# Kernel optimization log

Hardware: AMD Instinct MI355X
Metric: run time of the kernel (lower is better)

The kernel has to match this reference:

```python
import jax, jax.numpy as jnp
import numpy as np

V, D, H, L, F, S_MAX = 32000, 1024, 16, 6, 4, 1024
B, S = 2, 1024
HD = D // H  # head dim = 64


def setup_inputs() -> dict:
    key = jax.random.key(0)
    ks = jax.random.split(key, 8)
    init = lambda k, shape: jax.random.normal(k, shape, jnp.float32) * 0.02
    return dict(
        X=jax.random.randint(ks[0], (B, S), 0, V),
        tok_emb=init(ks[1], (V, D)),
        pos_emb=jnp.zeros((1, S_MAX, D), jnp.float32),  # initialized to zeros as in source
        qkv_w=init(ks[2], (D, 3 * D)), qkv_b=jnp.zeros((3 * D,), jnp.float32),
        out_w=init(ks[3], (D, D)), out_b=jnp.zeros((D,), jnp.float32),
        ln1_s=jnp.ones((D,), jnp.float32), ln1_b=jnp.zeros((D,), jnp.float32),
        ln2_s=jnp.ones((D,), jnp.float32), ln2_b=jnp.zeros((D,), jnp.float32),
        ff1_w=init(ks[4], (D, F * D)), ff1_b=jnp.zeros((F * D,), jnp.float32),
        ff2_w=init(ks[5], (F * D, D)), ff2_b=jnp.zeros((D,), jnp.float32),
        lnf_s=jnp.ones((D,), jnp.float32), lnf_b=jnp.zeros((D,), jnp.float32),
        head_w=init(ks[6], (D, V)), head_b=jnp.zeros((V,), jnp.float32),
    )


def _layernorm(x, scale, bias, eps=1e-5):
    m = x.mean(-1, keepdims=True)
    v = x.var(-1, keepdims=True)
    return (x - m) / jnp.sqrt(v + eps) * scale + bias


def _attention(x, qkv_w, qkv_b, out_w, out_b, mask):
    b, s, _ = x.shape
    qkv = (x @ qkv_w + qkv_b).reshape(b, s, H, 3 * HD)
    q, k, v = jnp.split(qkv, 3, axis=-1)  # each [b,s,H,HD]
    attn = jnp.einsum('bqhd,bkhd->bhqk', q, k) / jnp.sqrt(jnp.float32(HD))
    attn = jnp.where(mask, attn, -jnp.inf)
    attn = jax.nn.softmax(attn, axis=-1)
    out = jnp.einsum('bhqk,bkhd->bqhd', attn, v).reshape(b, s, D)
    return out @ out_w + out_b


def reference(X, tok_emb, pos_emb, qkv_w, qkv_b, out_w, out_b,
              ln1_s, ln1_b, ln2_s, ln2_b, ff1_w, ff1_b, ff2_w, ff2_b,
              lnf_s, lnf_b, head_w, head_b):
    s = X.shape[1]
    x = tok_emb[X] + pos_emb[:, :s, :]
    mask = jnp.tril(jnp.ones((s, s), bool))  # causal
    # NOTE: the source GPT reuses ONE shared GPTBlock for all layers.
    for _ in range(L):
        a = _attention(x, qkv_w, qkv_b, out_w, out_b, mask)
        x = _layernorm(x + a, ln1_s, ln1_b)
        f = jax.nn.gelu(x @ ff1_w + ff1_b, approximate=False) @ ff2_w + ff2_b
        x = _layernorm(x + f, ln2_s, ln2_b)
    x = _layernorm(x, lnf_s, lnf_b)
    logits = x @ head_w + head_b
    return jax.nn.softmax(logits, axis=-1)
```

## Files before the change

### kernel.cpp

```cpp
#include <hip/hip_runtime.h>
#include <math.h>

typedef unsigned short u16;
typedef short short8 __attribute__((ext_vector_type(8)));
typedef float floatx4 __attribute__((ext_vector_type(4)));

__device__ __forceinline__ u16 f2bf(float f) {
  unsigned int u = __float_as_uint(f);
  u += 0x7fffu + ((u >> 16) & 1u);
  return (u16)(u >> 16);
}

__device__ __forceinline__ void gld_lds16(const void* g, void* l) {
  __builtin_amdgcn_global_load_lds(
      (__attribute__((address_space(1))) void*)(g),
      (__attribute__((address_space(3))) void*)(l), 16, 0, 0);
}

__global__ __launch_bounds__(256) void transpose_all(
    const float* __restrict__ W0, u16* __restrict__ T0,
    const float* __restrict__ W1, u16* __restrict__ T1,
    const float* __restrict__ W2, u16* __restrict__ T2,
    const float* __restrict__ W3, u16* __restrict__ T3,
    const float* __restrict__ W4, u16* __restrict__ T4)
{
  int bid = blockIdx.x;
  const float* W; u16* Wt; int K, N, lb;
  if (bid < 3072)       { W = W0; Wt = T0; K = 1024; N = 3072;  lb = bid;         }
  else if (bid < 4096)  { W = W1; Wt = T1; K = 1024; N = 1024;  lb = bid - 3072;  }
  else if (bid < 8192)  { W = W2; Wt = T2; K = 1024; N = 4096;  lb = bid - 4096;  }
  else if (bid < 12288) { W = W3; Wt = T3; K = 4096; N = 1024;  lb = bid - 8192;  }
  else                  { W = W4; Wt = T4; K = 1024; N = 32000; lb = bid - 12288; }
  int nbx = N >> 5;
  int bx = lb % nbx, by = lb / nbx;

  __shared__ float tile[32][33];
  int tx = threadIdx.x & 31, ty = threadIdx.x >> 5;
  int n0 = bx * 32, k0 = by * 32;
#pragma unroll
  for (int i = 0; i < 4; i++)
    tile[ty + i * 8][tx] = W[(size_t)(k0 + ty + i * 8) * N + n0 + tx];
  __syncthreads();
#pragma unroll
  for (int i = 0; i < 4; i++)
    Wt[(size_t)(n0 + ty + i * 8) * K + k0 + tx] = f2bf(tile[tx][ty + i * 8]);
}

__global__ __launch_bounds__(256) void embed_kernel(
    const int* __restrict__ X, const float* __restrict__ tok,
    const float* __restrict__ pos, float* __restrict__ x, u16* __restrict__ xbf)
{
  int bs = blockIdx.x, t = threadIdx.x;
  int id = X[bs];
  int s = bs & 1023;
  float4 tv = *(const float4*)(tok + (size_t)id * 1024 + t * 4);
  float4 pv = *(const float4*)(pos + (size_t)s * 1024 + t * 4);
  float4 o;
  o.x = tv.x + pv.x; o.y = tv.y + pv.y; o.z = tv.z + pv.z; o.w = tv.w + pv.w;
  *(float4*)(x + (size_t)bs * 1024 + t * 4) = o;
  ushort4 ob; ob.x = f2bf(o.x); ob.y = f2bf(o.y); ob.z = f2bf(o.z); ob.w = f2bf(o.w);
  *(ushort4*)(xbf + (size_t)bs * 1024 + t * 4) = ob;
}

template<int BM, int WGC, int WTR, int WTC>
__global__ __launch_bounds__(256) void gemm_mfma(
    const u16* __restrict__ A, const u16* __restrict__ Bt,
    const float* __restrict__ bias, void* __restrict__ Cout,
    int M, int N, int K, int mode)
{
  constexpr int BN = WGC * WTC * 16;
  static_assert(BN == 128, "BN must be 128");
  __shared__ alignas(16) u16 As[BM * 64];
  __shared__ alignas(16) u16 Bs[128 * 64];

  const int t = threadIdx.x;
  const int wv = t >> 6, lane = t & 63;
  const int quad = lane >> 4, l16 = lane & 15;
  const int bx = blockIdx.x, by = blockIdx.y;
  const int row0 = by * BM, col0 = bx * BN;
  const int wr = (wv / WGC) * (WTR * 16);
  const int wc = (wv % WGC) * (WTC * 16);

  floatx4 acc[WTR][WTC];
#pragma unroll
  for (int i = 0; i < WTR; i++)
#pragma unroll
    for (int j = 0; j < WTC; j++) acc[i][j] = (floatx4){0.f, 0.f, 0.f, 0.f};

  const int srow = lane >> 3;
  const int scol = ((lane & 7) ^ srow) * 8;
  const int swz = l16 & 7;

  const u16* Abase = A + (size_t)row0 * K;
  const u16* Bbase = Bt + (size_t)col0 * K;
  constexpr int CA = BM / 32;
  constexpr int CB = 4;

  for (int k0 = 0; k0 < K; k0 += 64) {
#pragma unroll
    for (int i = 0; i < CA; i++) {
      int chunk = wv * CA + i;
      gld_lds16(Abase + (size_t)(chunk * 8 + srow) * K + k0 + scol, &As[chunk * 512]);
    }
#pragma unroll
    for (int i = 0; i < CB; i++) {
      int chunk = wv * CB + i;
      gld_lds16(Bbase + (size_t)(chunk * 8 + srow) * K + k0 + scol, &Bs[chunk * 512]);
    }
    __syncthreads();
#pragma unroll
    for (int ks = 0; ks < 64; ks += 32) {
      const int g = quad | (ks >> 3);
      const int cofs = ((g ^ swz) * 8);
      short8 a[WTR], b[WTC];
#pragma unroll
      for (int i = 0; i < WTR; i++)
        a[i] = *(const short8*)&As[(wr + i * 16 + l16) * 64 + cofs];
#pragma unroll
      for (int j = 0; j < WTC; j++)
        b[j] = *(const short8*)&Bs[(wc + j * 16 + l16) * 64 + cofs];
#pragma unroll
      for (int i = 0; i < WTR; i++)
#pragma unroll
        for (int j = 0; j < WTC; j++)
          acc[i][j] = __builtin_amdgcn_mfma_f32_16x16x32_bf16(a[i], b[j], acc[i][j], 0, 0, 0);
    }
    __syncthreads();
  }

#pragma unroll
  for (int i = 0; i < WTR; i++) {
    int rbase = row0 + wr + i * 16 + quad * 4;
#pragma unroll
    for (int j = 0; j < WTC; j++) {
      int c = col0 + wc + j * 16 + l16;
      float bv = bias[c];
#pragma unroll
      for (int r = 0; r < 4; r++) {
        float v = acc[i][j][r] + bv;
        size_t idx = (size_t)(rbase + r) * N + c;
        if (mode == 0) {
          ((float*)Cout)[idx] = v;
        } else if (mode == 1) {
          float gl = 0.5f * v * (1.f + erff(v * 0.70710678118f));
          ((u16*)Cout)[idx] = f2bf(gl);
        } else {
          ((u16*)Cout)[idx] = f2bf(v);
        }
      }
    }
  }
}

__global__ __launch_bounds__(512) void gemm_256_8ph(
    const u16* __restrict__ A, const u16* __restrict__ Bt,
    const float* __restrict__ bias, float* __restrict__ Cout,
    float2* __restrict__ partial, int M, int N, int K, int mode)
{
  __shared__ alignas(16) u16 As[2][256 * 64];
  __shared__ alignas(16) u16 Bs[2][256 * 64];

  const int t = threadIdx.x;
  const int wv = t >> 6, lane = t & 63;
  const int quad = lane >> 4, l16 = lane & 15;
  const int wm = wv >> 2, wn = wv & 3;

  int bx, by;
  {
    const int gx = (int)gridDim.x, gy = (int)gridDim.y;
    const int nwg = gx * gy;
    int hwid = (int)blockIdx.y * gx + (int)blockIdx.x;
    if ((nwg & 7) == 0) {
      int tl = (hwid & 7) * (nwg >> 3) + (hwid >> 3);
      bx = tl / gy; by = tl % gy;
    } else { bx = (int)blockIdx.x; by = (int)blockIdx.y; }
  }
  const int row0 = by * 256, col0 = bx * 256;

  const int srow = lane >> 3, lcol = lane & 7;
  const int scol = (lcol ^ srow) * 8;
  const int swz = l16 & 7;

  const u16* Abase = A + (size_t)row0 * K;
  const u16* Bbase = Bt + (size_t)col0 * K;
  const int NT = K >> 6;

  floatx4 acc[8][4];
#pragma unroll
  for (int i = 0; i < 8; i++)
#pragma unroll
    for (int j = 0; j < 4; j++) acc[i][j] = (floatx4){0.f, 0.f, 0.f, 0.f};

  auto stageA = [&](int b, int T, int mh) {
    const int kk = T * 64;
#pragma unroll
    for (int i = 0; i < 2; i++) {
      int ch = wv * 2 + i;
      int chunk = ((ch >> 3) * 16) + mh * 8 + (ch & 7);
      gld_lds16(Abase + (size_t)(chunk * 8 + srow) * K + kk + scol,
                &As[b][chunk * 512]);
    }
  };
  auto stageB = [&](int b, int T, int nh) {
    const int kk = T * 64;
#pragma unroll
    for (int i = 0; i < 2; i++) {
      int ch = wv * 2 + i;
      int chunk = ((ch >> 2) * 8) + nh * 4 + (ch & 3);
      gld_lds16(Bbase + (size_t)(chunk * 8 + srow) * K + kk + scol,
                &Bs[b][chunk * 512]);
    }
  };

  stageA(0, 0, 0); stageB(0, 0, 0); stageA(0, 0, 1); stageB(0, 0, 1);
  if (NT > 1) {
    stageA(1, 1, 0); stageB(1, 1, 0); stageA(1, 1, 1);
    asm volatile("s_waitcnt vmcnt(6)" ::: "memory");
  } else {
    asm volatile("s_waitcnt vmcnt(0)" ::: "memory");
  }
  __builtin_amdgcn_s_barrier();

  short8 af[4][2], bf0[2][2], bf1[2][2];
  for (int T = 0; T < NT; T++) {
    const int b = T & 1, bn = b ^ 1;

#pragma unroll
    for (int m = 0; m < 4; m++)
#pragma unroll
      for (int ks = 0; ks < 2; ks++) {
        int row = wm * 128 + m * 16 + l16;
        int g = quad + ks * 4;
        af[m][ks] = *(const short8*)&As[b][row * 64 + ((g ^ swz) * 8)];
      }
#pragma unroll
    for (int n = 0; n < 2; n++)
#pragma unroll
      for (int ks = 0; ks < 2; ks++) {
        int row = wn * 64 + n * 16 + l16;
        int g = quad + ks * 4;
        bf0[n][ks] = *(const short8*)&Bs[b][row * 64 + ((g ^ swz) * 8)];
      }
    if (T + 1 < NT) stageB(bn, T + 1, 1);
    asm volatile("" ::: "memory");
    __builtin_amdgcn_s_setprio(1);
#pragma unroll
    for (int m = 0; m < 4; m++)
#pragma unroll
      for (int n = 0; n < 2; n++)
#pragma unroll
        for (int ks = 0; ks < 2; ks++)
          acc[m][n] = __builtin_amdgcn_mfma_f32_16x16x32_bf16(af[m][ks], bf0[n][ks], acc[m][n], 0, 0, 0);
    __builtin_amdgcn_s_setprio(0);
    __builtin_amdgcn_s_barrier();

#pragma unroll
    for (int n = 0; n < 2; n++)
#pragma unroll
      for (int ks = 0; ks < 2; ks++) {
        int row = wn * 64 + 32 + n * 16 + l16;
        int g = quad + ks * 4;
        bf1[n][ks] = *(const short8*)&Bs[b][row * 64 + ((g ^ swz) * 8)];
      }
    if (T + 2 < NT) stageA(b, T + 2, 0);
    asm volatile("" ::: "memory");
    __builtin_amdgcn_s_setprio(1);
#pragma unroll
    for (int m = 0; m < 4; m++)
#pragma unroll
      for (int n = 0; n < 2; n++)
#pragma unroll
        for (int ks = 0; ks < 2; ks++)
          acc[m][2 + n] = __builtin_amdgcn_mfma_f32_16x16x32_bf16(af[m][ks], bf1[n][ks], acc[m][2 + n], 0, 0, 0);
    __builtin_amdgcn_s_setprio(0);
    __builtin_amdgcn_s_barrier();

#pragma unroll
    for (int m = 0; m < 4; m++)
#pragma unroll
      for (int ks = 0; ks < 2; ks++) {
        int row = wm * 128 + 64 + m * 16 + l16;
        int g = quad + ks * 4;
        af[m][ks] = *(const short8*)&As[b][row * 64 + ((g ^ swz) * 8)];
      }
    if (T + 2 < NT) stageB(b, T + 2, 0);
    asm volatile("" ::: "memory");
    __builtin_amdgcn_s_setprio(1);
#pragma unroll
    for (int m = 0; m < 4; m++)
#pragma unroll
      for (int n = 0; n < 2; n++)
#pragma unroll
        for (int ks = 0; ks < 2; ks++)
          acc[4 + m][n] = __builtin_amdgcn_mfma_f32_16x16x32_bf16(af[m][ks], bf0[n][ks], acc[4 + m][n], 0, 0, 0);
    __builtin_amdgcn_s_setprio(0);
    __builtin_amdgcn_s_barrier();

    if (T + 2 < NT) stageA(b, T + 2, 1);
    asm volatile("" ::: "memory");
    __builtin_amdgcn_s_setprio(1);
#pragma unroll
    for (int m = 0; m < 4; m++)
#pragma unroll
      for (int n = 0; n < 2; n++)
#pragma unroll
        for (int ks = 0; ks < 2; ks++)
          acc[4 + m][2 + n] = __builtin_amdgcn_mfma_f32_16x16x32_bf16(af[m][ks], bf1[n][ks], acc[4 + m][2 + n], 0, 0, 0);
    __builtin_amdgcn_s_setprio(0);
    if (T + 2 < NT) asm volatile("s_waitcnt vmcnt(6)" ::: "memory");
    else            asm volatile("s_waitcnt vmcnt(0)" ::: "memory");
    __builtin_amdgcn_s_barrier();
  }

  float* redm = (float*)&As[0][0];
  float* reds = redm + 256 * 4;

  float bvj[4];
#pragma unroll
  for (int j = 0; j < 4; j++)
    bvj[j] = bias[col0 + wn * 64 + (j >> 1) * 32 + (j & 1) * 16 + l16];

#pragma unroll
  for (int i = 0; i < 8; i++) {
    int rloc = wm * 128 + (i >> 2) * 64 + (i & 3) * 16 + quad * 4;
    int rbase = row0 + rloc;
    if (mode == 2) {
#pragma unroll
      for (int r = 0; r < 4; r++) {
        float vv[4];
        float mx = -3.0e38f;
#pragma unroll
        for (int j = 0; j < 4; j++) {
          int c = col0 + wn * 64 + (j >> 1) * 32 + (j & 1) * 16 + l16;
          float v = acc[i][j][r] + bvj[j];
          vv[j] = v;
          Cout[(size_t)(rbase + r) * N + c] = v;
          mx = fmaxf(mx, v);
        }
#pragma unroll
        for (int off = 1; off < 16; off <<= 1) mx = fmaxf(mx, __shfl_xor(mx, off, 64));
        float ss = 0.f;
#pragma unroll
        for (int j = 0; j < 4; j++) ss += __expf(vv[j] - mx);
#pragma unroll
        for (int off = 1; off < 16; off <<= 1) ss += __shfl_xor(ss, off, 64);
        if (l16 == 0) {
          redm[(rloc + r) * 4 + wn] = mx;
          reds[(rloc + r) * 4 + wn] = ss;
        }
      }
    } else {
#pragma unroll
      for (int j = 0; j < 4; j++) {
        int c = col0 + wn * 64 + (j >> 1) * 32 + (j & 1) * 16 + l16;
#pragma unroll
        for (int r = 0; r < 4; r++)
          Cout[(size_t)(rbase + r) * N + c] = acc[i][j][r] + bvj[j];
      }
    }
  }
  if (mode == 2) {
    __syncthreads();
    const int pnb = N >> 8;
    if (t < 256) {
      float M2 = redm[t * 4], S2 = reds[t * 4];
#pragma unroll
      for (int w = 1; w < 4; w++) {
        float m2 = redm[t * 4 + w], s2 = reds[t * 4 + w];
        float mn = fmaxf(M2, m2);
        S2 = S2 * __expf(M2 - mn) + s2 * __expf(m2 - mn);
        M2 = mn;
      }
      partial[(size_t)(row0 + t) * pnb + bx] = make_float2(M2, S2);
    }
  }
}

__global__ __launch_bounds__(256) void qkv_reshape(
    const u16* __restrict__ qkv, u16* __restrict__ Q, u16* __restrict__ K,
    u16* __restrict__ VT)
{
  __shared__ u16 tile[64][65];
  int st = blockIdx.x, h = blockIdx.y, b = blockIdx.z;
  int bh = b * 16 + h;
  int t = threadIdx.x;
  int row = t >> 2, c0 = (t & 3) * 16;
  const u16* src = qkv + (size_t)(b * 1024 + st * 64 + row) * 3072 + h * 192;

#pragma unroll
  for (int part = 0; part < 2; part++) {
    u16* dst = (part == 0 ? Q : K) + ((size_t)bh * 1024 + st * 64 + row) * 64 + c0;
    short8 v0 = *(const short8*)(src + part * 64 + c0);
    short8 v1 = *(const short8*)(src + part * 64 + c0 + 8);
    *(short8*)dst = v0;
    *(short8*)(dst + 8) = v1;
  }
  {
    short8 v0 = *(const short8*)(src + 128 + c0);
    short8 v1 = *(const short8*)(src + 128 + c0 + 8);
#pragma unroll
    for (int k = 0; k < 8; k++) {
      tile[row][c0 + k] = ((const u16*)&v0)[k];
      tile[row][c0 + 8 + k] = ((const u16*)&v1)[k];
    }
  }
  __syncthreads();
  u16* dst = VT + ((size_t)bh * 64 + row) * 1024 + st * 64 + c0;
  u16 ov[16];
#pragma unroll
  for (int k = 0; k < 16; k++) ov[k] = tile[c0 + k][row];
  *(short8*)dst = *(const short8*)&ov[0];
  *(short8*)(dst + 8) = *(const short8*)&ov[8];
}

__global__ __launch_bounds__(256) void flash_attn(
    const u16* __restrict__ Q, const u16* __restrict__ K,
    const u16* __restrict__ VT, u16* __restrict__ out)
{
  __shared__ alignas(16) u16 Ps[64][72];
  int qt = (int)gridDim.x - 1 - (int)blockIdx.x;
  int h = blockIdx.y, b = blockIdx.z;
  int bh = b * 16 + h;
  int t = threadIdx.x;
  int wv = t >> 6, lane = t & 63, l16 = lane & 15, quad = lane >> 4;
  int qrow0 = qt * 64 + wv * 16;

  const u16* Qb = Q + (size_t)bh * 1024 * 64;
  const u16* Kb = K + (size_t)bh * 1024 * 64;
  const u16* Vb = VT + (size_t)bh * 64 * 1024;

  short8 qfrag[2];
  qfrag[0] = *(const short8*)(Qb + (size_t)(qrow0 + l16) * 64 + quad * 8);
  qfrag[1] = *(const short8*)(Qb + (size_t)(qrow0 + l16) * 64 + 32 + quad * 8);

  floatx4 accO[4];
#pragma unroll
  for (int i = 0; i < 4; i++) accO[i] = (floatx4){0.f, 0.f, 0.f, 0.f};
  float m[4], l[4];
#pragma unroll
  for (int r = 0; r < 4; r++) { m[r] = -3.0e38f; l[r] = 0.f; }

  for (int jt = 0; jt <= qt; jt++) {
    const u16* Kt = Kb + (size_t)(jt * 64) * 64;
    float sv[4][4];
    bool diag = (jt == qt);
#pragma unroll
    for (int nt = 0; nt < 4; nt++) {
      short8 b0 = *(const short8*)(Kt + (size_t)(nt * 16 + l16) * 64 + quad * 8);
      short8 b1 = *(const short8*)(Kt + (size_t)(nt * 16 + l16) * 64 + 32 + quad * 8);
      floatx4 acc = (floatx4){0.f, 0.f, 0.f, 0.f};
      acc = __builtin_amdgcn_mfma_f32_16x16x32_bf16(qfrag[0], b0, acc, 0, 0, 0);
      acc = __builtin_amdgcn_mfma_f32_16x16x32_bf16(qfrag[1], b1, acc, 0, 0, 0);
#pragma unroll
      for (int r = 0; r < 4; r++) {
        float v = acc[r] * 0.125f;
        if (diag) {
          int j = nt * 16 + l16;
          int q = wv * 16 + quad * 4 + r;
          if (j > q) v = -3.0e38f;
        }
        sv[nt][r] = v;
      }
    }
    float rm[4];
#pragma unroll
    for (int r = 0; r < 4; r++) {
      rm[r] = fmaxf(fmaxf(sv[0][r], sv[1][r]), fmaxf(sv[2][r], sv[3][r]));
#pragma unroll
      for (int off = 1; off < 16; off <<= 1)
        rm[r] = fmaxf(rm[r], __shfl_xor(rm[r], off, 64));
    }
    float al[4], rs[4];
    float p[4][4];
#pragma unroll
    for (int r = 0; r < 4; r++) {
      float mn = fmaxf(m[r], rm[r]);
      al[r] = __expf(m[r] - mn);
      m[r] = mn;
      rs[r] = 0.f;
    }
#pragma unroll
    for (int nt = 0; nt < 4; nt++)
#pragma unroll
      for (int r = 0; r < 4; r++) {
        float e = __expf(sv[nt][r] - m[r]);
        p[nt][r] = e;
        rs[r] += e;
      }
#pragma unroll
    for (int r = 0; r < 4; r++) {
#pragma unroll
      for (int off = 1; off < 16; off <<= 1)
        rs[r] += __shfl_xor(rs[r], off, 64);
      l[r] = l[r] * al[r] + rs[r];
    }
#pragma unroll
    for (int nt = 0; nt < 4; nt++)
#pragma unroll
      for (int r = 0; r < 4; r++) accO[nt][r] *= al[r];

    __syncthreads();
#pragma unroll
    for (int nt = 0; nt < 4; nt++)
#pragma unroll
      for (int r = 0; r < 4; r++)
        Ps[wv * 16 + quad * 4 + r][nt * 16 + l16] = f2bf(p[nt][r]);
    __syncthreads();

    short8 pf0 = *(const short8*)&Ps[wv * 16 + l16][quad * 8];
    short8 pf1 = *(const short8*)&Ps[wv * 16 + l16][32 + quad * 8];
#pragma unroll
    for (int nt = 0; nt < 4; nt++) {
      const u16* Vt = Vb + (size_t)(nt * 16 + l16) * 1024 + jt * 64;
      short8 v0 = *(const short8*)(Vt + quad * 8);
      short8 v1 = *(const short8*)(Vt + 32 + quad * 8);
      accO[nt] = __builtin_amdgcn_mfma_f32_16x16x32_bf16(pf0, v0, accO[nt], 0, 0, 0);
      accO[nt] = __builtin_amdgcn_mfma_f32_16x16x32_bf16(pf1, v1, accO[nt], 0, 0, 0);
    }
  }

  float inv[4];
#pragma unroll
  for (int r = 0; r < 4; r++) inv[r] = 1.f / l[r];
  __syncthreads();
#pragma unroll
  for (int nt = 0; nt < 4; nt++)
#pragma unroll
    for (int r = 0; r < 4; r++)
      Ps[wv * 16 + quad * 4 + r][nt * 16 + l16] = f2bf(accO[nt][r] * inv[r]);
  __syncthreads();
  int r = t >> 2, c0 = (t & 3) * 16;
  short8 o0 = *(const short8*)&Ps[r][c0];
  short8 o1 = *(const short8*)&Ps[r][c0 + 8];
  u16* dst = out + (size_t)(b * 1024 + qt * 64 + r) * 1024 + h * 64 + c0;
  *(short8*)dst = o0;
  *(short8*)(dst + 8) = o1;
}

__global__ __launch_bounds__(256) void ln_kernel(
    const float* __restrict__ xin, const float* __restrict__ add,
    const float* __restrict__ sc, const float* __restrict__ bi,
    float* __restrict__ xout, u16* __restrict__ xbf)
{
  int row = blockIdx.x, t = threadIdx.x;
  float4 v = *(const float4*)(xin + (size_t)row * 1024 + t * 4);
  if (add) {
    float4 a = *(const float4*)(add + (size_t)row * 1024 + t * 4);
    v.x += a.x; v.y += a.y; v.z += a.z; v.w += a.w;
  }
  float s1 = v.x + v.y + v.z + v.w;
  float s2 = v.x * v.x + v.y * v.y + v.z * v.z + v.w * v.w;
#pragma unroll
  for (int off = 32; off > 0; off >>= 1) {
    s1 += __shfl_down(s1, off);
    s2 += __shfl_down(s2, off);
  }
  __shared__ float r1[4], r2[4];
  int lane = t & 63, wv = t >> 6;
  if (lane == 0) { r1[wv] = s1; r2[wv] = s2; }
  __syncthreads();
  float S1 = r1[0] + r1[1] + r1[2] + r1[3];
  float S2 = r2[0] + r2[1] + r2[2] + r2[3];
  float mn = S1 * (1.f / 1024.f);
  float var = S2 * (1.f / 1024.f) - mn * mn;
  float inv = rsqrtf(var + 1e-5f);
  float4 sv = *(const float4*)(sc + t * 4);
  float4 bv = *(const float4*)(bi + t * 4);
  float4 o;
  o.x = (v.x - mn) * inv * sv.x + bv.x;
  o.y = (v.y - mn) * inv * sv.y + bv.y;
  o.z = (v.z - mn) * inv * sv.z + bv.z;
  o.w = (v.w - mn) * inv * sv.w + bv.w;
  *(float4*)(xout + (size_t)row * 1024 + t * 4) = o;
  ushort4 ob; ob.x = f2bf(o.x); ob.y = f2bf(o.y); ob.z = f2bf(o.z); ob.w = f2bf(o.w);
  *(ushort4*)(xbf + (size_t)row * 1024 + t * 4) = ob;
}

__global__ __launch_bounds__(256) void softmax_final(
    float* __restrict__ out, const float2* __restrict__ partial, int pnb)
{
  int row = blockIdx.x, t = threadIdx.x;
  float m = -3.0e38f, s = 0.f;
  for (int j = t; j < pnb; j += 256) {
    float2 p = partial[(size_t)row * pnb + j];
    float mn = fmaxf(m, p.x);
    s = s * __expf(m - mn) + p.y * __expf(p.x - mn);
    m = mn;
  }
#pragma unroll
  for (int off = 32; off > 0; off >>= 1) {
    float m2 = __shfl_down(m, off), s2 = __shfl_down(s, off);
    float mn = fmaxf(m, m2);
    s = s * __expf(m - mn) + s2 * __expf(m2 - mn);
    m = mn;
  }
  __shared__ float rm[4], rs[4];
  int lane = t & 63, wv = t >> 6;
  if (lane == 0) { rm[wv] = m; rs[wv] = s; }
  __syncthreads();
  float M = rm[0], S = rs[0];
#pragma unroll
  for (int i = 1; i < 4; i++) {
    float mn = fmaxf(M, rm[i]);
    S = S * __expf(M - mn) + rs[i] * __expf(rm[i] - mn);
    M = mn;
  }
  float inv = 1.f / S;
  float4* p4 = (float4*)(out + (size_t)row * 32000);
  for (int j = t; j < 8000; j += 256) {
    float4 v = p4[j];
    v.x = __expf(v.x - M) * inv;
    v.y = __expf(v.y - M) * inv;
    v.z = __expf(v.z - M) * inv;
    v.w = __expf(v.w - M) * inv;
    p4[j] = v;
  }
}

extern "C" void kernel_launch(void* const* d_in, const int* in_sizes, int n_in,
                              void* d_out, int out_size, void* d_ws, size_t ws_size,
                              hipStream_t stream)
{
  const int*   X       = (const int*)d_in[0];
  const float* tok_emb = (const float*)d_in[1];
  const float* pos_emb = (const float*)d_in[2];
  const float* qkv_w   = (const float*)d_in[3];
  const float* qkv_b   = (const float*)d_in[4];
  const float* out_w   = (const float*)d_in[5];
  const float* out_b   = (const float*)d_in[6];
  const float* ln1_s   = (const float*)d_in[7];
  const float* ln1_b   = (const float*)d_in[8];
  const float* ln2_s   = (const float*)d_in[9];
  const float* ln2_b   = (const float*)d_in[10];
  const float* ff1_w   = (const float*)d_in[11];
  const float* ff1_b   = (const float*)d_in[12];
  const float* ff2_w   = (const float*)d_in[13];
  const float* ff2_b   = (const float*)d_in[14];
  const float* lnf_s   = (const float*)d_in[15];
  const float* lnf_b   = (const float*)d_in[16];
  const float* head_w  = (const float*)d_in[17];
  const float* head_b  = (const float*)d_in[18];

  char* ws = (char*)d_ws;
  float* x      = (float*)ws;            ws += 2048ull * 1024 * 4;
  u16*   xbf    = (u16*)ws;              ws += 2048ull * 1024 * 2;
  u16*   qkvbuf = (u16*)ws;              ws += 2048ull * 3072 * 4;
  u16*   attnbf = (u16*)ws;              ws += 2048ull * 1024 * 2;
  float* tmp    = (float*)ws;            ws += 2048ull * 1024 * 4;
  u16*   hbf    = (u16*)ws;              ws += 2048ull * 4096 * 2;
  u16*   qkvT   = (u16*)ws;              ws += 3072ull * 1024 * 2;
  u16*   outT   = (u16*)ws;              ws += 1024ull * 1024 * 2;
  u16*   ff1T   = (u16*)ws;              ws += 4096ull * 1024 * 2;
  u16*   ff2T   = (u16*)ws;              ws += 1024ull * 4096 * 2;
  u16*   headT  = (u16*)ws;              ws += 32000ull * 1024 * 2;
  float2* smpart = (float2*)ws;          ws += 2048ull * 250 * 8;

  u16* Qbf = hbf;
  u16* Kbf = hbf + 2048ull * 1024;
  u16* VTb = hbf + 2 * 2048ull * 1024;

  transpose_all<<<dim3(44288), 256, 0, stream>>>(
      qkv_w, qkvT, out_w, outT, ff1_w, ff1T, ff2_w, ff2T, head_w, headT);

  embed_kernel<<<2048, 256, 0, stream>>>(X, tok_emb, pos_emb, x, xbf);

  for (int l = 0; l < 6; l++) {
    gemm_mfma<128, 2, 4, 4><<<dim3(3072 / 128, 2048 / 128), 256, 0, stream>>>(
        xbf, qkvT, qkv_b, qkvbuf, 2048, 3072, 1024, 3);
    qkv_reshape<<<dim3(16, 16, 2), 256, 0, stream>>>(qkvbuf, Qbf, Kbf, VTb);
    flash_attn<<<dim3(16, 16, 2), 256, 0, stream>>>(Qbf, Kbf, VTb, attnbf);
    gemm_mfma<64, 4, 4, 2><<<dim3(1024 / 128, 2048 / 64), 256, 0, stream>>>(
        attnbf, outT, out_b, tmp, 2048, 1024, 1024, 0);
    ln_kernel<<<2048, 256, 0, stream>>>(x, tmp, ln1_s, ln1_b, x, xbf);
    gemm_mfma<128, 2, 4, 4><<<dim3(4096 / 128, 2048 / 128), 256, 0, stream>>>(
        xbf, ff1T, ff1_b, hbf, 2048, 4096, 1024, 1);
    gemm_mfma<64, 4, 4, 2><<<dim3(1024 / 128, 2048 / 64), 256, 0, stream>>>(
        hbf, ff2T, ff2_b, tmp, 2048, 1024, 4096, 0);
    ln_kernel<<<2048, 256, 0, stream>>>(x, tmp, ln2_s, ln2_b, x, xbf);
  }

  ln_kernel<<<2048, 256, 0, stream>>>(x, nullptr, lnf_s, lnf_b, x, xbf);
  gemm_256_8ph<<<dim3(32000 / 256, 2048 / 256), 512, 0, stream>>>(
      xbf, headT, head_b, (float*)d_out, smpart, 2048, 32000, 1024, 2);
  softmax_final<<<2048, 256, 0, stream>>>((float*)d_out, smpart, 125);
}
```

Baseline: 2.124 ms.

## Fuse QKV reshape into GEMM epilogue and replace head GEMM with generic kernel

```diff
diff --git a/kernel.cpp b/kernel.cpp
--- a/kernel.cpp
+++ b/kernel.cpp
@@ -66,6 +66,7 @@
 __global__ __launch_bounds__(256) void gemm_mfma(
     const u16* __restrict__ A, const u16* __restrict__ Bt,
     const float* __restrict__ bias, void* __restrict__ Cout,
+    float2* __restrict__ partial, u16* __restrict__ VTout,
     int M, int N, int K, int mode)
 {
   constexpr int BN = WGC * WTC * 16;
@@ -80,6 +81,7 @@
   const int row0 = by * BM, col0 = bx * BN;
   const int wr = (wv / WGC) * (WTR * 16);
   const int wc = (wv % WGC) * (WTC * 16);
+  const int wcid = wv % WGC;
 
   floatx4 acc[WTR][WTC];
 #pragma unroll
@@ -128,294 +130,105 @@
     __syncthreads();
   }
 
-#pragma unroll
-  for (int i = 0; i < WTR; i++) {
-    int rbase = row0 + wr + i * 16 + quad * 4;
-#pragma unroll
-    for (int j = 0; j < WTC; j++) {
-      int c = col0 + wc + j * 16 + l16;
-      float bv = bias[c];
+  float bvj[WTC];
+#pragma unroll
+  for (int j = 0; j < WTC; j++) bvj[j] = bias[col0 + wc + j * 16 + l16];
+
+  if (mode == 2) {
+    float* redm = (float*)As;
+    float* reds = redm + BM * WGC;
+#pragma unroll
+    for (int i = 0; i < WTR; i++) {
+      int rloc = wr + i * 16 + quad * 4;
+      int rbase = row0 + rloc;
 #pragma unroll
       for (int r = 0; r < 4; r++) {
-        float v = acc[i][j][r] + bv;
-        size_t idx = (size_t)(rbase + r) * N + c;
-        if (mode == 0) {
-          ((float*)Cout)[idx] = v;
-        } else if (mode == 1) {
-          float gl = 0.5f * v * (1.f + erff(v * 0.70710678118f));
-          ((u16*)Cout)[idx] = f2bf(gl);
-        } else {
-          ((u16*)Cout)[idx] = f2bf(v);
-        }
-      }
-    }
-  }
-}
-
-__global__ __launch_bounds__(512) void gemm_256_8ph(
-    const u16* __restrict__ A, const u16* __restrict__ Bt,
-    const float* __restrict__ bias, float* __restrict__ Cout,
-    float2* __restrict__ partial, int M, int N, int K, int mode)
-{
-  __shared__ alignas(16) u16 As[2][256 * 64];
-  __shared__ alignas(16) u16 Bs[2][256 * 64];
-
-  const int t = threadIdx.x;
-  const int wv = t >> 6, lane = t & 63;
-  const int quad = lane >> 4, l16 = lane & 15;
-  const int wm = wv >> 2, wn = wv & 3;
-
-  int bx, by;
-  {
-    const int gx = (int)gridDim.x, gy = (int)gridDim.y;
-    const int nwg = gx * gy;
-    int hwid = (int)blockIdx.y * gx + (int)blockIdx.x;
-    if ((nwg & 7) == 0) {
-      int tl = (hwid & 7) * (nwg >> 3) + (hwid >> 3);
-      bx = tl / gy; by = tl % gy;
-    } else { bx = (int)blockIdx.x; by = (int)blockIdx.y; }
-  }
-  const int row0 = by * 256, col0 = bx * 256;
-
-  const int srow = lane >> 3, lcol = lane & 7;
-  const int scol = (lcol ^ srow) * 8;
-  const int swz = l16 & 7;
-
-  const u16* Abase = A + (size_t)row0 * K;
-  const u16* Bbase = Bt + (size_t)col0 * K;
-  const int NT = K >> 6;
-
-  floatx4 acc[8][4];
-#pragma unroll
-  for (int i = 0; i < 8; i++)
-#pragma unroll
-    for (int j = 0; j < 4; j++) acc[i][j] = (floatx4){0.f, 0.f, 0.f, 0.f};
-
-  auto stageA = [&](int b, int T, int mh) {
-    const int kk = T * 64;
-#pragma unroll
-    for (int i = 0; i < 2; i++) {
-      int ch = wv * 2 + i;
-      int chunk = ((ch >> 3) * 16) + mh * 8 + (ch & 7);
-      gld_lds16(Abase + (size_t)(chunk * 8 + srow) * K + kk + scol,
-                &As[b][chunk * 512]);
-    }
-  };
-  auto stageB = [&](int b, int T, int nh) {
-    const int kk = T * 64;
-#pragma unroll
-    for (int i = 0; i < 2; i++) {
-      int ch = wv * 2 + i;
-      int chunk = ((ch >> 2) * 8) + nh * 4 + (ch & 3);
-      gld_lds16(Bbase + (size_t)(chunk * 8 + srow) * K + kk + scol,
-                &Bs[b][chunk * 512]);
-    }
-  };
-
-  stageA(0, 0, 0); stageB(0, 0, 0); stageA(0, 0, 1); stageB(0, 0, 1);
-  if (NT > 1) {
-    stageA(1, 1, 0); stageB(1, 1, 0); stageA(1, 1, 1);
-    asm volatile("s_waitcnt vmcnt(6)" ::: "memory");
-  } else {
-    asm volatile("s_waitcnt vmcnt(0)" ::: "memory");
-  }
-  __builtin_amdgcn_s_barrier();
-
-  short8 af[4][2], bf0[2][2], bf1[2][2];
-  for (int T = 0; T < NT; T++) {
-    const int b = T & 1, bn = b ^ 1;
-
-#pragma unroll
-    for (int m = 0; m < 4; m++)
-#pragma unroll
-      for (int ks = 0; ks < 2; ks++) {
-        int row = wm * 128 + m * 16 + l16;
-        int g = quad + ks * 4;
-        af[m][ks] = *(const short8*)&As[b][row * 64 + ((g ^ swz) * 8)];
-      }
-#pragma unroll
-    for (int n = 0; n < 2; n++)
-#pragma unroll
-      for (int ks = 0; ks < 2; ks++) {
-        int row = wn * 64 + n * 16 + l16;
-        int g = quad + ks * 4;
-        bf0[n][ks] = *(const short8*)&Bs[b][row * 64 + ((g ^ swz) * 8)];
-      }
-    if (T + 1 < NT) stageB(bn, T + 1, 1);
-    asm volatile("" ::: "memory");
-    __builtin_amdgcn_s_setprio(1);
-#pragma unroll
-    for (int m = 0; m < 4; m++)
-#pragma unroll
-      for (int n = 0; n < 2; n++)
-#pragma unroll
-        for (int ks = 0; ks < 2; ks++)
-          acc[m][n] = __builtin_amdgcn_mfma_f32_16x16x32_bf16(af[m][ks], bf0[n][ks], acc[m][n], 0, 0, 0);
-    __builtin_amdgcn_s_setprio(0);
-    __builtin_amdgcn_s_barrier();
-
-#pragma unroll
-    for (int n = 0; n < 2; n++)
-#pragma unroll
-      for (int ks = 0; ks < 2; ks++) {
-        int row = wn * 64 + 32 + n * 16 + l16;
-        int g = quad + ks * 4;
-        bf1[n][ks] = *(const short8*)&Bs[b][row * 64 + ((g ^ swz) * 8)];
-      }
-    if (T + 2 < NT) stageA(b, T + 2, 0);
-    asm volatile("" ::: "memory");
-    __builtin_amdgcn_s_setprio(1);
-#pragma unroll
-    for (int m = 0; m < 4; m++)
-#pragma unroll
-      for (int n = 0; n < 2; n++)
-#pragma unroll
-        for (int ks = 0; ks < 2; ks++)
-          acc[m][2 + n] = __builtin_amdgcn_mfma_f32_16x16x32_bf16(af[m][ks], bf1[n][ks], acc[m][2 + n], 0, 0, 0);
-    __builtin_amdgcn_s_setprio(0);
-    __builtin_amdgcn_s_barrier();
-
-#pragma unroll
-    for (int m = 0; m < 4; m++)
-#pragma unroll
-      for (int ks = 0; ks < 2; ks++) {
-        int row = wm * 128 + 64 + m * 16 + l16;
-        int g = quad + ks * 4;
-        af[m][ks] = *(const short8*)&As[b][row * 64 + ((g ^ swz) * 8)];
-      }
-    if (T + 2 < NT) stageB(b, T + 2, 0);
-    asm volatile("" ::: "memory");
-    __builtin_amdgcn_s_setprio(1);
-#pragma unroll
-    for (int m = 0; m < 4; m++)
-#pragma unroll
-      for (int n = 0; n < 2; n++)
-#pragma unroll
-        for (int ks = 0; ks < 2; ks++)
-          acc[4 + m][n] = __builtin_amdgcn_mfma_f32_16x16x32_bf16(af[m][ks], bf0[n][ks], acc[4 + m][n], 0, 0, 0);
-    __builtin_amdgcn_s_setprio(0);
-    __builtin_amdgcn_s_barrier();
-
-    if (T + 2 < NT) stageA(b, T + 2, 1);
-    asm volatile("" ::: "memory");
-    __builtin_amdgcn_s_setprio(1);
-#pragma unroll
-    for (int m = 0; m < 4; m++)
-#pragma unroll
-      for (int n = 0; n < 2; n++)
-#pragma unroll
-        for (int ks = 0; ks < 2; ks++)
-          acc[4 + m][2 + n] = __builtin_amdgcn_mfma_f32_16x16x32_bf16(af[m][ks], bf1[n][ks], acc[4 + m][2 + n], 0, 0, 0);
-    __builtin_amdgcn_s_setprio(0);
-    if (T + 2 < NT) asm volatile("s_waitcnt vmcnt(6)" ::: "memory");
-    else            asm volatile("s_waitcnt vmcnt(0)" ::: "memory");
-    __builtin_amdgcn_s_barrier();
-  }
-
-  float* redm = (float*)&As[0][0];
-  float* reds = redm + 256 * 4;
-
-  float bvj[4];
-#pragma unroll
-  for (int j = 0; j < 4; j++)
-    bvj[j] = bias[col0 + wn * 64 + (j >> 1) * 32 + (j & 1) * 16 + l16];
-
-#pragma unroll
-  for (int i = 0; i < 8; i++) {
-    int rloc = wm * 128 + (i >> 2) * 64 + (i & 3) * 16 + quad * 4;
-    int rbase = row0 + rloc;
-    if (mode == 2) {
-#pragma unroll
-      for (int r = 0; r < 4; r++) {
-        float vv[4];
+        float vv[WTC];
         float mx = -3.0e38f;
 #pragma unroll
-        for (int j = 0; j < 4; j++) {
-          int c = col0 + wn * 64 + (j >> 1) * 32 + (j & 1) * 16 + l16;
+        for (int j = 0; j < WTC; j++) {
+          int c = col0 + wc + j * 16 + l16;
           float v = acc[i][j][r] + bvj[j];
           vv[j] = v;
-          Cout[(size_t)(rbase + r) * N + c] = v;
+          ((float*)Cout)[(size_t)(rbase + r) * N + c] = v;
           mx = fmaxf(mx, v);
         }
 #pragma unroll
         for (int off = 1; off < 16; off <<= 1) mx = fmaxf(mx, __shfl_xor(mx, off, 64));
         float ss = 0.f;
 #pragma unroll
-        for (int j = 0; j < 4; j++) ss += __expf(vv[j] - mx);
+        for (int j = 0; j < WTC; j++) ss += __expf(vv[j] - mx);
 #pragma unroll
         for (int off = 1; off < 16; off <<= 1) ss += __shfl_xor(ss, off, 64);
         if (l16 == 0) {
-          redm[(rloc + r) * 4 + wn] = mx;
-          reds[(rloc + r) * 4 + wn] = ss;
+          redm[(rloc + r) * WGC + wcid] = mx;
+          reds[(rloc + r) * WGC + wcid] = ss;
         }
       }
-    } else {
-#pragma unroll
-      for (int j = 0; j < 4; j++) {
-        int c = col0 + wn * 64 + (j >> 1) * 32 + (j & 1) * 16 + l16;
-#pragma unroll
-        for (int r = 0; r < 4; r++)
-          Cout[(size_t)(rbase + r) * N + c] = acc[i][j][r] + bvj[j];
-      }
-    }
-  }
-  if (mode == 2) {
+    }
     __syncthreads();
-    const int pnb = N >> 8;
-    if (t < 256) {
-      float M2 = redm[t * 4], S2 = reds[t * 4];
-#pragma unroll
-      for (int w = 1; w < 4; w++) {
-        float m2 = redm[t * 4 + w], s2 = reds[t * 4 + w];
+    const int pnb = N / BN;
+    for (int rr = t; rr < BM; rr += 256) {
+      float M2 = redm[rr * WGC], S2 = reds[rr * WGC];
+#pragma unroll
+      for (int w = 1; w < WGC; w++) {
+        float m2 = redm[rr * WGC + w], s2 = reds[rr * WGC + w];
         float mn = fmaxf(M2, m2);
         S2 = S2 * __expf(M2 - mn) + s2 * __expf(m2 - mn);
         M2 = mn;
       }
-      partial[(size_t)(row0 + t) * pnb + bx] = make_float2(M2, S2);
-    }
-  }
-}
-
-__global__ __launch_bounds__(256) void qkv_reshape(
-    const u16* __restrict__ qkv, u16* __restrict__ Q, u16* __restrict__ K,
-    u16* __restrict__ VT)
-{
-  __shared__ u16 tile[64][65];
-  int st = blockIdx.x, h = blockIdx.y, b = blockIdx.z;
-  int bh = b * 16 + h;
-  int t = threadIdx.x;
-  int row = t >> 2, c0 = (t & 3) * 16;
-  const u16* src = qkv + (size_t)(b * 1024 + st * 64 + row) * 3072 + h * 192;
-
-#pragma unroll
-  for (int part = 0; part < 2; part++) {
-    u16* dst = (part == 0 ? Q : K) + ((size_t)bh * 1024 + st * 64 + row) * 64 + c0;
-    short8 v0 = *(const short8*)(src + part * 64 + c0);
-    short8 v1 = *(const short8*)(src + part * 64 + c0 + 8);
-    *(short8*)dst = v0;
-    *(short8*)(dst + 8) = v1;
-  }
-  {
-    short8 v0 = *(const short8*)(src + 128 + c0);
-    short8 v1 = *(const short8*)(src + 128 + c0 + 8);
-#pragma unroll
-    for (int k = 0; k < 8; k++) {
-      tile[row][c0 + k] = ((const u16*)&v0)[k];
-      tile[row][c0 + 8 + k] = ((const u16*)&v1)[k];
-    }
-  }
-  __syncthreads();
-  u16* dst = VT + ((size_t)bh * 64 + row) * 1024 + st * 64 + c0;
-  u16 ov[16];
-#pragma unroll
-  for (int k = 0; k < 16; k++) ov[k] = tile[c0 + k][row];
-  *(short8*)dst = *(const short8*)&ov[0];
-  *(short8*)(dst + 8) = *(const short8*)&ov[8];
+      partial[(size_t)(row0 + rr) * pnb + bx] = make_float2(M2, S2);
+    }
+  } else if (mode == 4) {
+#pragma unroll
+    for (int i = 0; i < WTR; i++) {
+      int rbase = row0 + wr + i * 16 + quad * 4;
+#pragma unroll
+      for (int j = 0; j < WTC; j++) {
+        int c = col0 + wc + j * 16 + l16;
+        int h = c / 192, within = c - h * 192;
+        if (within < 128) {
+#pragma unroll
+          for (int r = 0; r < 4; r++)
+            ((u16*)Cout)[(size_t)(rbase + r) * N + c] = f2bf(acc[i][j][r] + bvj[j]);
+        } else {
+          int d = within - 128;
+          int bb = rbase >> 10, s0 = rbase & 1023;
+          ushort4 ov;
+          ov.x = f2bf(acc[i][j][0] + bvj[j]);
+          ov.y = f2bf(acc[i][j][1] + bvj[j]);
+          ov.z = f2bf(acc[i][j][2] + bvj[j]);
+          ov.w = f2bf(acc[i][j][3] + bvj[j]);
+          *(ushort4*)(VTout + ((size_t)(bb * 16 + h) * 64 + d) * 1024 + s0) = ov;
+        }
+      }
+    }
+  } else {
+#pragma unroll
+    for (int i = 0; i < WTR; i++) {
+      int rbase = row0 + wr + i * 16 + quad * 4;
+#pragma unroll
+      for (int j = 0; j < WTC; j++) {
+        int c = col0 + wc + j * 16 + l16;
+#pragma unroll
+        for (int r = 0; r < 4; r++) {
+          float v = acc[i][j][r] + bvj[j];
+          size_t idx = (size_t)(rbase + r) * N + c;
+          if (mode == 0) {
+            ((float*)Cout)[idx] = v;
+          } else {
+            float gl = 0.5f * v * (1.f + erff(v * 0.70710678118f));
+            ((u16*)Cout)[idx] = f2bf(gl);
+          }
+        }
+      }
+    }
+  }
 }
 
 __global__ __launch_bounds__(256) void flash_attn(
-    const u16* __restrict__ Q, const u16* __restrict__ K,
-    const u16* __restrict__ VT, u16* __restrict__ out)
+    const u16* __restrict__ qkv, const u16* __restrict__ VT,
+    u16* __restrict__ out)
 {
   __shared__ alignas(16) u16 Ps[64][72];
   int qt = (int)gridDim.x - 1 - (int)blockIdx.x;
@@ -425,13 +238,13 @@
   int wv = t >> 6, lane = t & 63, l16 = lane & 15, quad = lane >> 4;
   int qrow0 = qt * 64 + wv * 16;
 
-  const u16* Qb = Q + (size_t)bh * 1024 * 64;
-  const u16* Kb = K + (size_t)bh * 1024 * 64;
+  const u16* Qb = qkv + (size_t)b * 1024 * 3072 + h * 192;
+  const u16* Kb = Qb + 64;
   const u16* Vb = VT + (size_t)bh * 64 * 1024;
 
   short8 qfrag[2];
-  qfrag[0] = *(const short8*)(Qb + (size_t)(qrow0 + l16) * 64 + quad * 8);
-  qfrag[1] = *(const short8*)(Qb + (size_t)(qrow0 + l16) * 64 + 32 + quad * 8);
+  qfrag[0] = *(const short8*)(Qb + (size_t)(qrow0 + l16) * 3072 + quad * 8);
+  qfrag[1] = *(const short8*)(Qb + (size_t)(qrow0 + l16) * 3072 + 32 + quad * 8);
 
   floatx4 accO[4];
 #pragma unroll
@@ -441,13 +254,13 @@
   for (int r = 0; r < 4; r++) { m[r] = -3.0e38f; l[r] = 0.f; }
 
   for (int jt = 0; jt <= qt; jt++) {
-    const u16* Kt = Kb + (size_t)(jt * 64) * 64;
     float sv[4][4];
     bool diag = (jt == qt);
 #pragma unroll
     for (int nt = 0; nt < 4; nt++) {
-      short8 b0 = *(const short8*)(Kt + (size_t)(nt * 16 + l16) * 64 + quad * 8);
-      short8 b1 = *(const short8*)(Kt + (size_t)(nt * 16 + l16) * 64 + 32 + quad * 8);
+      const u16* Kt = Kb + (size_t)(jt * 64 + nt * 16 + l16) * 3072;
+      short8 b0 = *(const short8*)(Kt + quad * 8);
+      short8 b1 = *(const short8*)(Kt + 32 + quad * 8);
       floatx4 acc = (floatx4){0.f, 0.f, 0.f, 0.f};
       acc = __builtin_amdgcn_mfma_f32_16x16x32_bf16(qfrag[0], b0, acc, 0, 0, 0);
       acc = __builtin_amdgcn_mfma_f32_16x16x32_bf16(qfrag[1], b1, acc, 0, 0, 0);
@@ -644,7 +457,8 @@
   char* ws = (char*)d_ws;
   float* x      = (float*)ws;            ws += 2048ull * 1024 * 4;
   u16*   xbf    = (u16*)ws;              ws += 2048ull * 1024 * 2;
-  u16*   qkvbuf = (u16*)ws;              ws += 2048ull * 3072 * 4;
+  u16*   qkvbuf = (u16*)ws;              ws += 2048ull * 3072 * 2;
+  u16*   VTb    = (u16*)ws;              ws += 32ull * 64 * 1024 * 2;
   u16*   attnbf = (u16*)ws;              ws += 2048ull * 1024 * 2;
   float* tmp    = (float*)ws;            ws += 2048ull * 1024 * 4;
   u16*   hbf    = (u16*)ws;              ws += 2048ull * 4096 * 2;
@@ -655,10 +469,6 @@
   u16*   headT  = (u16*)ws;              ws += 32000ull * 1024 * 2;
   float2* smpart = (float2*)ws;          ws += 2048ull * 250 * 8;
 
-  u16* Qbf = hbf;
-  u16* Kbf = hbf + 2048ull * 1024;
-  u16* VTb = hbf + 2 * 2048ull * 1024;
-
   transpose_all<<<dim3(44288), 256, 0, stream>>>(
       qkv_w, qkvT, out_w, outT, ff1_w, ff1T, ff2_w, ff2T, head_w, headT);
 
@@ -666,21 +476,20 @@
 
   for (int l = 0; l < 6; l++) {
     gemm_mfma<128, 2, 4, 4><<<dim3(3072 / 128, 2048 / 128), 256, 0, stream>>>(
-        xbf, qkvT, qkv_b, qkvbuf, 2048, 3072, 1024, 3);
-    qkv_reshape<<<dim3(16, 16, 2), 256, 0, stream>>>(qkvbuf, Qbf, Kbf, VTb);
-    flash_attn<<<dim3(16, 16, 2), 256, 0, stream>>>(Qbf, Kbf, VTb, attnbf);
+        xbf, qkvT, qkv_b, qkvbuf, nullptr, VTb, 2048, 3072, 1024, 4);
+    flash_attn<<<dim3(16, 16, 2), 256, 0, stream>>>(qkvbuf, VTb, attnbf);
     gemm_mfma<64, 4, 4, 2><<<dim3(1024 / 128, 2048 / 64), 256, 0, stream>>>(
-        attnbf, outT, out_b, tmp, 2048, 1024, 1024, 0);
+        attnbf, outT, out_b, tmp, nullptr, nullptr, 2048, 1024, 1024, 0);
     ln_kernel<<<2048, 256, 0, stream>>>(x, tmp, ln1_s, ln1_b, x, xbf);
     gemm_mfma<128, 2, 4, 4><<<dim3(4096 / 128, 2048 / 128), 256, 0, stream>>>(
-        xbf, ff1T, ff1_b, hbf, 2048, 4096, 1024, 1);
+        xbf, ff1T, ff1_b, hbf, nullptr, nullptr, 2048, 4096, 1024, 1);
     gemm_mfma<64, 4, 4, 2><<<dim3(1024 / 128, 2048 / 64), 256, 0, stream>>>(
-        hbf, ff2T, ff2_b, tmp, 2048, 1024, 4096, 0);
+        hbf, ff2T, ff2_b, tmp, nullptr, nullptr, 2048, 1024, 4096, 0);
     ln_kernel<<<2048, 256, 0, stream>>>(x, tmp, ln2_s, ln2_b, x, xbf);
   }
 
   ln_kernel<<<2048, 256, 0, stream>>>(x, nullptr, lnf_s, lnf_b, x, xbf);
-  gemm_256_8ph<<<dim3(32000 / 256, 2048 / 256), 512, 0, stream>>>(
-      xbf, headT, head_b, (float*)d_out, smpart, 2048, 32000, 1024, 2);
-  softmax_final<<<2048, 256, 0, stream>>>((float*)d_out, smpart, 125);
-}
+  gemm_mfma<128, 2, 4, 4><<<dim3(32000 / 128, 2048 / 128), 256, 0, stream>>>(
+      xbf, headT, head_b, (float*)d_out, smpart, nullptr, 2048, 32000, 1024, 2);
+  softmax_final<<<2048, 256, 0, stream>>>((float*)d_out, smpart, 250);
+}
```

New measurement: 2.177 ms. 2.5% more time.

## Fuse QKV reshape into GEMM epilogue and shrink N tile for D-output GEMMs

Applied to the files above, without the earlier changes.

```diff
diff --git a/kernel.cpp b/kernel.cpp
--- a/kernel.cpp
+++ b/kernel.cpp
@@ -66,12 +66,13 @@
 __global__ __launch_bounds__(256) void gemm_mfma(
     const u16* __restrict__ A, const u16* __restrict__ Bt,
     const float* __restrict__ bias, void* __restrict__ Cout,
+    u16* __restrict__ VTout,
     int M, int N, int K, int mode)
 {
   constexpr int BN = WGC * WTC * 16;
-  static_assert(BN == 128, "BN must be 128");
+  static_assert(BN == 128 || BN == 64, "BN must be 64 or 128");
   __shared__ alignas(16) u16 As[BM * 64];
-  __shared__ alignas(16) u16 Bs[128 * 64];
+  __shared__ alignas(16) u16 Bs[BN * 64];
 
   const int t = threadIdx.x;
   const int wv = t >> 6, lane = t & 63;
@@ -94,7 +95,7 @@
   const u16* Abase = A + (size_t)row0 * K;
   const u16* Bbase = Bt + (size_t)col0 * K;
   constexpr int CA = BM / 32;
-  constexpr int CB = 4;
+  constexpr int CB = BN / 32;
 
   for (int k0 = 0; k0 < K; k0 += 64) {
 #pragma unroll
@@ -128,24 +129,51 @@
     __syncthreads();
   }
 
-#pragma unroll
-  for (int i = 0; i < WTR; i++) {
-    int rbase = row0 + wr + i * 16 + quad * 4;
-#pragma unroll
-    for (int j = 0; j < WTC; j++) {
-      int c = col0 + wc + j * 16 + l16;
-      float bv = bias[c];
-#pragma unroll
-      for (int r = 0; r < 4; r++) {
-        float v = acc[i][j][r] + bv;
-        size_t idx = (size_t)(rbase + r) * N + c;
-        if (mode == 0) {
-          ((float*)Cout)[idx] = v;
-        } else if (mode == 1) {
-          float gl = 0.5f * v * (1.f + erff(v * 0.70710678118f));
-          ((u16*)Cout)[idx] = f2bf(gl);
+  float bvj[WTC];
+#pragma unroll
+  for (int j = 0; j < WTC; j++) bvj[j] = bias[col0 + wc + j * 16 + l16];
+
+  if (mode == 4) {
+#pragma unroll
+    for (int i = 0; i < WTR; i++) {
+      int rbase = row0 + wr + i * 16 + quad * 4;
+#pragma unroll
+      for (int j = 0; j < WTC; j++) {
+        int c = col0 + wc + j * 16 + l16;
+        int h = c / 192, within = c - h * 192;
+        if (within < 128) {
+#pragma unroll
+          for (int r = 0; r < 4; r++)
+            ((u16*)Cout)[(size_t)(rbase + r) * N + c] = f2bf(acc[i][j][r] + bvj[j]);
         } else {
-          ((u16*)Cout)[idx] = f2bf(v);
+          int d = within - 128;
+          int bb = rbase >> 10, s0 = rbase & 1023;
+          ushort4 ov;
+          ov.x = f2bf(acc[i][j][0] + bvj[j]);
+          ov.y = f2bf(acc[i][j][1] + bvj[j]);
+          ov.z = f2bf(acc[i][j][2] + bvj[j]);
+          ov.w = f2bf(acc[i][j][3] + bvj[j]);
+          *(ushort4*)(VTout + ((size_t)(bb * 16 + h) * 64 + d) * 1024 + s0) = ov;
+        }
+      }
+    }
+  } else {
+#pragma unroll
+    for (int i = 0; i < WTR; i++) {
+      int rbase = row0 + wr + i * 16 + quad * 4;
+#pragma unroll
+      for (int j = 0; j < WTC; j++) {
+        int c = col0 + wc + j * 16 + l16;
+#pragma unroll
+        for (int r = 0; r < 4; r++) {
+          float v = acc[i][j][r] + bvj[j];
+          size_t idx = (size_t)(rbase + r) * N + c;
+          if (mode == 0) {
+            ((float*)Cout)[idx] = v;
+          } else {
+            float gl = 0.5f * v * (1.f + erff(v * 0.70710678118f));
+            ((u16*)Cout)[idx] = f2bf(gl);
+          }
         }
       }
     }
@@ -376,46 +404,9 @@
   }
 }
 
-__global__ __launch_bounds__(256) void qkv_reshape(
-    const u16* __restrict__ qkv, u16* __restrict__ Q, u16* __restrict__ K,
-    u16* __restrict__ VT)
-{
-  __shared__ u16 tile[64][65];
-  int st = blockIdx.x, h = blockIdx.y, b = blockIdx.z;
-  int bh = b * 16 + h;
-  int t = threadIdx.x;
-  int row = t >> 2, c0 = (t & 3) * 16;
-  const u16* src = qkv + (size_t)(b * 1024 + st * 64 + row) * 3072 + h * 192;
-
-#pragma unroll
-  for (int part = 0; part < 2; part++) {
-    u16* dst = (part == 0 ? Q : K) + ((size_t)bh * 1024 + st * 64 + row) * 64 + c0;
-    short8 v0 = *(const short8*)(src + part * 64 + c0);
-    short8 v1 = *(const short8*)(src + part * 64 + c0 + 8);
-    *(short8*)dst = v0;
-    *(short8*)(dst + 8) = v1;
-  }
-  {
-    short8 v0 = *(const short8*)(src + 128 + c0);
-    short8 v1 = *(const short8*)(src + 128 + c0 + 8);
-#pragma unroll
-    for (int k = 0; k < 8; k++) {
-      tile[row][c0 + k] = ((const u16*)&v0)[k];
-      tile[row][c0 + 8 + k] = ((const u16*)&v1)[k];
-    }
-  }
-  __syncthreads();
-  u16* dst = VT + ((size_t)bh * 64 + row) * 1024 + st * 64 + c0;
-  u16 ov[16];
-#pragma unroll
-  for (int k = 0; k < 16; k++) ov[k] = tile[c0 + k][row];
-  *(short8*)dst = *(const short8*)&ov[0];
-  *(short8*)(dst + 8) = *(const short8*)&ov[8];
-}
-
 __global__ __launch_bounds__(256) void flash_attn(
-    const u16* __restrict__ Q, const u16* __restrict__ K,
-    const u16* __restrict__ VT, u16* __restrict__ out)
+    const u16* __restrict__ qkv, const u16* __restrict__ VT,
+    u16* __restrict__ out)
 {
   __shared__ alignas(16) u16 Ps[64][72];
   int qt = (int)gridDim.x - 1 - (int)blockIdx.x;
@@ -425,13 +416,13 @@
   int wv = t >> 6, lane = t & 63, l16 = lane & 15, quad = lane >> 4;
   int qrow0 = qt * 64 + wv * 16;
 
-  const u16* Qb = Q + (size_t)bh * 1024 * 64;
-  const u16* Kb = K + (size_t)bh * 1024 * 64;
+  const u16* Qb = qkv + (size_t)b * 1024 * 3072 + h * 192;
+  const u16* Kb = Qb + 64;
   const u16* Vb = VT + (size_t)bh * 64 * 1024;
 
   short8 qfrag[2];
-  qfrag[0] = *(const short8*)(Qb + (size_t)(qrow0 + l16) * 64 + quad * 8);
-  qfrag[1] = *(const short8*)(Qb + (size_t)(qrow0 + l16) * 64 + 32 + quad * 8);
+  qfrag[0] = *(const short8*)(Qb + (size_t)(qrow0 + l16) * 3072 + quad * 8);
+  qfrag[1] = *(const short8*)(Qb + (size_t)(qrow0 + l16) * 3072 + 32 + quad * 8);
 
   floatx4 accO[4];
 #pragma unroll
@@ -441,13 +432,13 @@
   for (int r = 0; r < 4; r++) { m[r] = -3.0e38f; l[r] = 0.f; }
 
   for (int jt = 0; jt <= qt; jt++) {
-    const u16* Kt = Kb + (size_t)(jt * 64) * 64;
     float sv[4][4];
     bool diag = (jt == qt);
 #pragma unroll
     for (int nt = 0; nt < 4; nt++) {
-      short8 b0 = *(const short8*)(Kt + (size_t)(nt * 16 + l16) * 64 + quad * 8);
-      short8 b1 = *(const short8*)(Kt + (size_t)(nt * 16 + l16) * 64 + 32 + quad * 8);
+      const u16* Kt = Kb + (size_t)(jt * 64 + nt * 16 + l16) * 3072;
+      short8 b0 = *(const short8*)(Kt + quad * 8);
+      short8 b1 = *(const short8*)(Kt + 32 + quad * 8);
       floatx4 acc = (floatx4){0.f, 0.f, 0.f, 0.f};
       acc = __builtin_amdgcn_mfma_f32_16x16x32_bf16(qfrag[0], b0, acc, 0, 0, 0);
       acc = __builtin_amdgcn_mfma_f32_16x16x32_bf16(qfrag[1], b1, acc, 0, 0, 0);
@@ -644,7 +635,8 @@
   char* ws = (char*)d_ws;
   float* x      = (float*)ws;            ws += 2048ull * 1024 * 4;
   u16*   xbf    = (u16*)ws;              ws += 2048ull * 1024 * 2;
-  u16*   qkvbuf = (u16*)ws;              ws += 2048ull * 3072 * 4;
+  u16*   qkvbuf = (u16*)ws;              ws += 2048ull * 3072 * 2;
+  u16*   VTb    = (u16*)ws;              ws += 32ull * 64 * 1024 * 2;
   u16*   attnbf = (u16*)ws;              ws += 2048ull * 1024 * 2;
   float* tmp    = (float*)ws;            ws += 2048ull * 1024 * 4;
   u16*   hbf    = (u16*)ws;              ws += 2048ull * 4096 * 2;
@@ -655,10 +647,6 @@
   u16*   headT  = (u16*)ws;              ws += 32000ull * 1024 * 2;
   float2* smpart = (float2*)ws;          ws += 2048ull * 250 * 8;
 
-  u16* Qbf = hbf;
-  u16* Kbf = hbf + 2048ull * 1024;
-  u16* VTb = hbf + 2 * 2048ull * 1024;
-
   transpose_all<<<dim3(44288), 256, 0, stream>>>(
       qkv_w, qkvT, out_w, outT, ff1_w, ff1T, ff2_w, ff2T, head_w, headT);
 
@@ -666,16 +654,15 @@
 
   for (int l = 0; l < 6; l++) {
     gemm_mfma<128, 2, 4, 4><<<dim3(3072 / 128, 2048 / 128), 256, 0, stream>>>(
-        xbf, qkvT, qkv_b, qkvbuf, 2048, 3072, 1024, 3);
-    qkv_reshape<<<dim3(16, 16, 2), 256, 0, stream>>>(qkvbuf, Qbf, Kbf, VTb);
-    flash_attn<<<dim3(16, 16, 2), 256, 0, stream>>>(Qbf, Kbf, VTb, attnbf);
-    gemm_mfma<64, 4, 4, 2><<<dim3(1024 / 128, 2048 / 64), 256, 0, stream>>>(
-        attnbf, outT, out_b, tmp, 2048, 1024, 1024, 0);
+        xbf, qkvT, qkv_b, qkvbuf, VTb, 2048, 3072, 1024, 4);
+    flash_attn<<<dim3(16, 16, 2), 256, 0, stream>>>(qkvbuf, VTb, attnbf);
+    gemm_mfma<64, 4, 4, 1><<<dim3(1024 / 64, 2048 / 64), 256, 0, stream>>>(
+        attnbf, outT, out_b, tmp, nullptr, 2048, 1024, 1024, 0);
     ln_kernel<<<2048, 256, 0, stream>>>(x, tmp, ln1_s, ln1_b, x, xbf);
     gemm_mfma<128, 2, 4, 4><<<dim3(4096 / 128, 2048 / 128), 256, 0, stream>>>(
-        xbf, ff1T, ff1_b, hbf, 2048, 4096, 1024, 1);
-    gemm_mfma<64, 4, 4, 2><<<dim3(1024 / 128, 2048 / 64), 256, 0, stream>>>(
-        hbf, ff2T, ff2_b, tmp, 2048, 1024, 4096, 0);
+        xbf, ff1T, ff1_b, hbf, nullptr, 2048, 4096, 1024, 1);
+    gemm_mfma<64, 4, 4, 1><<<dim3(1024 / 64, 2048 / 64), 256, 0, stream>>>(
+        hbf, ff2T, ff2_b, tmp, nullptr, 2048, 1024, 4096, 0);
     ln_kernel<<<2048, 256, 0, stream>>>(x, tmp, ln2_s, ln2_b, x, xbf);
   }
 
```

Measured after the change: 1.972 ms. 1.08x faster.
